# Kernel tuning notes

Measured on AMD Instinct MI355X. Metric: run time of the kernel, lower is better.

The kernel has to match this reference:

```python
import jax, jax.numpy as jnp
import numpy as np

TEMPERATURE = 0.3


def setup_inputs() -> dict:
    key = jax.random.key(0)
    k1, k2, k3 = jax.random.split(key, 3)
    B, C = 65536, 1000
    logits = jax.random.normal(k1, (B, C), dtype=jnp.float32)
    targets = jax.random.randint(k2, (B,), 0, C, dtype=jnp.int64)
    similarity_matrix = jax.random.uniform(k3, (C, C), dtype=jnp.float32)
    return {"logits": logits, "targets": targets, "similarity_matrix": similarity_matrix}


def reference(logits, targets, similarity_matrix):
    # Gather per-sample similarity rows: [B, C]
    sim_rows = similarity_matrix[targets]
    # soft_targets = normalized exp(-sim/T) == softmax(-sim/T) along classes
    soft_targets = jax.nn.softmax(-sim_rows / TEMPERATURE, axis=1)
    log_probs = jax.nn.log_softmax(logits, axis=1)
    loss = -(soft_targets * log_probs).sum(axis=1).mean()
    return loss
```

## Files before the change

kernel.cpp:

```cpp
#include <hip/hip_runtime.h>
#include <math.h>


#define TEMPERATURE 0.3f
#define C_DIM 1000
#define LOSS_BLOCKS 2048

__device__ __forceinline__ float waveAllSum(float v) {
    #pragma unroll
    for (int m = 1; m < 64; m <<= 1) v += __shfl_xor(v, m, 64);
    return v;
}

__global__ void soft_targets_kernel(const float* __restrict__ sim,
                                    float* __restrict__ P) {
    const int wid  = threadIdx.x >> 6;
    const int lane = threadIdx.x & 63;
    const int c = blockIdx.x * 4 + wid;

    const float4* row  = (const float4*)(sim + (size_t)c * C_DIM);
    float4*       prow = (float4*)(P + (size_t)c * C_DIM);

    const bool tail = lane < 58;
    const int  i3   = tail ? lane + 192 : lane;

    float4 v0 = row[lane];
    float4 v1 = row[lane + 64];
    float4 v2 = row[lane + 128];
    float4 v3 = row[i3];

    const float s = -1.0f / TEMPERATURE;
    float4 e0, e1, e2, e3;
    e0.x = __expf(v0.x * s); e0.y = __expf(v0.y * s); e0.z = __expf(v0.z * s); e0.w = __expf(v0.w * s);
    e1.x = __expf(v1.x * s); e1.y = __expf(v1.y * s); e1.z = __expf(v1.z * s); e1.w = __expf(v1.w * s);
    e2.x = __expf(v2.x * s); e2.y = __expf(v2.y * s); e2.z = __expf(v2.z * s); e2.w = __expf(v2.w * s);
    e3.x = __expf(v3.x * s); e3.y = __expf(v3.y * s); e3.z = __expf(v3.z * s); e3.w = __expf(v3.w * s);

    float sum = (e0.x + e0.y + e0.z + e0.w)
              + (e1.x + e1.y + e1.z + e1.w)
              + (e2.x + e2.y + e2.z + e2.w)
              + (tail ? (e3.x + e3.y + e3.z + e3.w) : 0.0f);
    sum = waveAllSum(sum);
    const float inv = 1.0f / sum;

    prow[lane]       = make_float4(e0.x * inv, e0.y * inv, e0.z * inv, e0.w * inv);
    prow[lane + 64]  = make_float4(e1.x * inv, e1.y * inv, e1.z * inv, e1.w * inv);
    prow[lane + 128] = make_float4(e2.x * inv, e2.y * inv, e2.z * inv, e2.w * inv);
    if (tail)
        prow[lane + 192] = make_float4(e3.x * inv, e3.y * inv, e3.z * inv, e3.w * inv);
}

__global__ void loss_kernel(const float* __restrict__ logits,
                            const int* __restrict__ targets,
                            const float* __restrict__ P,
                            float* __restrict__ partials,
                            int B) {
    const int wid  = threadIdx.x >> 6;
    const int lane = threadIdx.x & 63;
    const int wave   = blockIdx.x * 4 + wid;
    const int nwaves = gridDim.x * 4;

    const bool tail = lane < 58;
    const int  i3   = tail ? lane + 192 : lane;

    float local = 0.0f;

    for (int i = wave; i < B; i += nwaves) {
        const int t = targets[i];
        const float4* lrow = (const float4*)(logits + (size_t)i * C_DIM);
        const float4* prow = (const float4*)(P + (size_t)t * C_DIM);

        float4 a0 = lrow[lane];
        float4 a1 = lrow[lane + 64];
        float4 a2 = lrow[lane + 128];
        float4 a3 = lrow[i3];
        float4 p0 = prow[lane];
        float4 p1 = prow[lane + 64];
        float4 p2 = prow[lane + 128];
        float4 p3 = prow[i3];

        float es = (__expf(a0.x) + __expf(a0.y) + __expf(a0.z) + __expf(a0.w))
                 + (__expf(a1.x) + __expf(a1.y) + __expf(a1.z) + __expf(a1.w))
                 + (__expf(a2.x) + __expf(a2.y) + __expf(a2.z) + __expf(a2.w));
        float es3 = __expf(a3.x) + __expf(a3.y) + __expf(a3.z) + __expf(a3.w);

        float dt = a0.x * p0.x + a0.y * p0.y + a0.z * p0.z + a0.w * p0.w
                 + a1.x * p1.x + a1.y * p1.y + a1.z * p1.z + a1.w * p1.w
                 + a2.x * p2.x + a2.y * p2.y + a2.z * p2.z + a2.w * p2.w;
        float dt3 = a3.x * p3.x + a3.y * p3.y + a3.z * p3.z + a3.w * p3.w;

        if (tail) { es += es3; dt += dt3; }

        es = waveAllSum(es);
        dt = waveAllSum(dt);

        local += __logf(es) - dt;
    }

    __shared__ float sloc[4];
    if (lane == 0) sloc[wid] = local;
    __syncthreads();
    if (threadIdx.x == 0)
        partials[blockIdx.x] = sloc[0] + sloc[1] + sloc[2] + sloc[3];
}

__global__ void finalize_kernel(const float* __restrict__ partials,
                                float* __restrict__ out, float invB) {
    const int wid  = threadIdx.x >> 6;
    const int lane = threadIdx.x & 63;
    float v = 0.0f;
    for (int i = threadIdx.x; i < LOSS_BLOCKS; i += 256) v += partials[i];
    v = waveAllSum(v);
    __shared__ float s[4];
    if (lane == 0) s[wid] = v;
    __syncthreads();
    if (threadIdx.x == 0) out[0] = (s[0] + s[1] + s[2] + s[3]) * invB;
}

extern "C" void kernel_launch(void* const* d_in, const int* in_sizes, int n_in,
                              void* d_out, int out_size, void* d_ws, size_t ws_size,
                              hipStream_t stream) {
    const float* logits  = (const float*)d_in[0];
    const int*   targets = (const int*)d_in[1];
    const float* sim     = (const float*)d_in[2];
    float* out = (float*)d_out;

    float* P        = (float*)d_ws;
    float* partials = (float*)d_ws + C_DIM * C_DIM;

    const int B = in_sizes[1];

    soft_targets_kernel<<<250, 256, 0, stream>>>(sim, P);
    loss_kernel<<<LOSS_BLOCKS, 256, 0, stream>>>(logits, targets, P, partials, B);
    finalize_kernel<<<1, 256, 0, stream>>>(partials, out, 1.0f / (float)B);
}
```

Before: 366.1 us.

## Unroll loss loop by two, defer dot reduction, nontemporal logits, atomic finalize

The loss loop now handles two samples per iteration so more loads are in flight. The per-sample dot-product reduction is replaced by one reduction at the end of each wave. Logits are read with nontemporal loads so the similarity-probability table stays cached. The finalize kernel is dropped in favour of an atomicAdd into a memset output, which removes a launch but makes the float summation order nondeterministic.

```diff
diff --git a/kernel.cpp b/kernel.cpp
--- a/kernel.cpp
+++ b/kernel.cpp
@@ -5,6 +5,8 @@
 #define TEMPERATURE 0.3f
 #define C_DIM 1000
 #define LOSS_BLOCKS 2048
+
+typedef float f4 __attribute__((ext_vector_type(4)));
 
 __device__ __forceinline__ float waveAllSum(float v) {
     #pragma unroll
@@ -18,19 +20,19 @@
     const int lane = threadIdx.x & 63;
     const int c = blockIdx.x * 4 + wid;
 
-    const float4* row  = (const float4*)(sim + (size_t)c * C_DIM);
-    float4*       prow = (float4*)(P + (size_t)c * C_DIM);
+    const f4* row  = (const f4*)(sim + (size_t)c * C_DIM);
+    f4*       prow = (f4*)(P + (size_t)c * C_DIM);
 
     const bool tail = lane < 58;
     const int  i3   = tail ? lane + 192 : lane;
 
-    float4 v0 = row[lane];
-    float4 v1 = row[lane + 64];
-    float4 v2 = row[lane + 128];
-    float4 v3 = row[i3];
+    f4 v0 = row[lane];
+    f4 v1 = row[lane + 64];
+    f4 v2 = row[lane + 128];
+    f4 v3 = row[i3];
 
     const float s = -1.0f / TEMPERATURE;
-    float4 e0, e1, e2, e3;
+    f4 e0, e1, e2, e3;
     e0.x = __expf(v0.x * s); e0.y = __expf(v0.y * s); e0.z = __expf(v0.z * s); e0.w = __expf(v0.w * s);
     e1.x = __expf(v1.x * s); e1.y = __expf(v1.y * s); e1.z = __expf(v1.z * s); e1.w = __expf(v1.w * s);
     e2.x = __expf(v2.x * s); e2.y = __expf(v2.y * s); e2.z = __expf(v2.z * s); e2.w = __expf(v2.w * s);
@@ -43,18 +45,48 @@
     sum = waveAllSum(sum);
     const float inv = 1.0f / sum;
 
-    prow[lane]       = make_float4(e0.x * inv, e0.y * inv, e0.z * inv, e0.w * inv);
-    prow[lane + 64]  = make_float4(e1.x * inv, e1.y * inv, e1.z * inv, e1.w * inv);
-    prow[lane + 128] = make_float4(e2.x * inv, e2.y * inv, e2.z * inv, e2.w * inv);
-    if (tail)
-        prow[lane + 192] = make_float4(e3.x * inv, e3.y * inv, e3.z * inv, e3.w * inv);
+    prow[lane]       = e0 * inv;
+    prow[lane + 64]  = e1 * inv;
+    prow[lane + 128] = e2 * inv;
+    if (tail) prow[lane + 192] = e3 * inv;
+}
+
+__device__ __forceinline__ void sample_body(const float* __restrict__ logits,
+                                            const float* __restrict__ P,
+                                            int i, int t, int lane, int i3, bool tail,
+                                            float& es_out, float& acc_dt) {
+    const f4* lrow = (const f4*)(logits + (size_t)i * C_DIM);
+    const f4* prow = (const f4*)(P + (size_t)t * C_DIM);
+
+    f4 a0 = __builtin_nontemporal_load(lrow + lane);
+    f4 a1 = __builtin_nontemporal_load(lrow + lane + 64);
+    f4 a2 = __builtin_nontemporal_load(lrow + lane + 128);
+    f4 a3 = __builtin_nontemporal_load(lrow + i3);
+    f4 p0 = prow[lane];
+    f4 p1 = prow[lane + 64];
+    f4 p2 = prow[lane + 128];
+    f4 p3 = prow[i3];
+
+    float es = (__expf(a0.x) + __expf(a0.y) + __expf(a0.z) + __expf(a0.w))
+             + (__expf(a1.x) + __expf(a1.y) + __expf(a1.z) + __expf(a1.w))
+             + (__expf(a2.x) + __expf(a2.y) + __expf(a2.z) + __expf(a2.w));
+    float es3 = __expf(a3.x) + __expf(a3.y) + __expf(a3.z) + __expf(a3.w);
+
+    float dt = a0.x * p0.x + a0.y * p0.y + a0.z * p0.z + a0.w * p0.w
+             + a1.x * p1.x + a1.y * p1.y + a1.z * p1.z + a1.w * p1.w
+             + a2.x * p2.x + a2.y * p2.y + a2.z * p2.z + a2.w * p2.w;
+    float dt3 = a3.x * p3.x + a3.y * p3.y + a3.z * p3.z + a3.w * p3.w;
+
+    if (tail) { es += es3; dt += dt3; }
+    es_out = es;
+    acc_dt += dt;
 }
 
 __global__ void loss_kernel(const float* __restrict__ logits,
                             const int* __restrict__ targets,
                             const float* __restrict__ P,
-                            float* __restrict__ partials,
-                            int B) {
+                            float* __restrict__ out,
+                            float invB, int B) {
     const int wid  = threadIdx.x >> 6;
     const int lane = threadIdx.x & 63;
     const int wave   = blockIdx.x * 4 + wid;
@@ -63,58 +95,36 @@
     const bool tail = lane < 58;
     const int  i3   = tail ? lane + 192 : lane;
 
-    float local = 0.0f;
+    float acc_log = 0.0f;
+    float acc_dt  = 0.0f;
 
-    for (int i = wave; i < B; i += nwaves) {
+    int i = wave;
+    for (; i + nwaves < B; i += 2 * nwaves) {
+        const int ta = targets[i];
+        const int tb = targets[i + nwaves];
+        float esA, esB;
+        sample_body(logits, P, i,          ta, lane, i3, tail, esA, acc_dt);
+        sample_body(logits, P, i + nwaves, tb, lane, i3, tail, esB, acc_dt);
+        esA = waveAllSum(esA);
+        esB = waveAllSum(esB);
+        acc_log += __logf(esA) + __logf(esB);
+    }
+    for (; i < B; i += nwaves) {
         const int t = targets[i];
-        const float4* lrow = (const float4*)(logits + (size_t)i * C_DIM);
-        const float4* prow = (const float4*)(P + (size_t)t * C_DIM);
-
-        float4 a0 = lrow[lane];
-        float4 a1 = lrow[lane + 64];
-        float4 a2 = lrow[lane + 128];
-        float4 a3 = lrow[i3];
-        float4 p0 = prow[lane];
-        float4 p1 = prow[lane + 64];
-        float4 p2 = prow[lane + 128];
-        float4 p3 = prow[i3];
-
-        float es = (__expf(a0.x) + __expf(a0.y) + __expf(a0.z) + __expf(a0.w))
-                 + (__expf(a1.x) + __expf(a1.y) + __expf(a1.z) + __expf(a1.w))
-                 + (__expf(a2.x) + __expf(a2.y) + __expf(a2.z) + __expf(a2.w));
-        float es3 = __expf(a3.x) + __expf(a3.y) + __expf(a3.z) + __expf(a3.w);
-
-        float dt = a0.x * p0.x + a0.y * p0.y + a0.z * p0.z + a0.w * p0.w
-                 + a1.x * p1.x + a1.y * p1.y + a1.z * p1.z + a1.w * p1.w
-                 + a2.x * p2.x + a2.y * p2.y + a2.z * p2.z + a2.w * p2.w;
-        float dt3 = a3.x * p3.x + a3.y * p3.y + a3.z * p3.z + a3.w * p3.w;
-
-        if (tail) { es += es3; dt += dt3; }
-
+        float es;
+        sample_body(logits, P, i, t, lane, i3, tail, es, acc_dt);
         es = waveAllSum(es);
-        dt = waveAllSum(dt);
-
-        local += __logf(es) - dt;
+        acc_log += __logf(es);
     }
 
+    const float dt_total = waveAllSum(acc_dt);
     __shared__ float sloc[4];
-    if (lane == 0) sloc[wid] = local;
+    if (lane == 0) sloc[wid] = acc_log - dt_total;
     __syncthreads();
-    if (threadIdx.x == 0)
-        partials[blockIdx.x] = sloc[0] + sloc[1] + sloc[2] + sloc[3];
-}
-
-__global__ void finalize_kernel(const float* __restrict__ partials,
-                                float* __restrict__ out, float invB) {
-    const int wid  = threadIdx.x >> 6;
-    const int lane = threadIdx.x & 63;
-    float v = 0.0f;
-    for (int i = threadIdx.x; i < LOSS_BLOCKS; i += 256) v += partials[i];
-    v = waveAllSum(v);
-    __shared__ float s[4];
-    if (lane == 0) s[wid] = v;
-    __syncthreads();
-    if (threadIdx.x == 0) out[0] = (s[0] + s[1] + s[2] + s[3]) * invB;
+    if (threadIdx.x == 0) {
+        const float blk = sloc[0] + sloc[1] + sloc[2] + sloc[3];
+        atomicAdd(out, blk * invB);
+    }
 }
 
 extern "C" void kernel_launch(void* const* d_in, const int* in_sizes, int n_in,
@@ -124,13 +134,12 @@
     const int*   targets = (const int*)d_in[1];
     const float* sim     = (const float*)d_in[2];
     float* out = (float*)d_out;
-
-    float* P        = (float*)d_ws;
-    float* partials = (float*)d_ws + C_DIM * C_DIM;
+    float* P   = (float*)d_ws;
 
     const int B = in_sizes[1];
 
+    hipMemsetAsync(out, 0, sizeof(float), stream);
     soft_targets_kernel<<<250, 256, 0, stream>>>(sim, P);
-    loss_kernel<<<LOSS_BLOCKS, 256, 0, stream>>>(logits, targets, P, partials, B);
-    finalize_kernel<<<1, 256, 0, stream>>>(partials, out, 1.0f / (float)B);
+    loss_kernel<<<LOSS_BLOCKS, 256, 0, stream>>>(logits, targets, P, out,
+                                                 1.0f / (float)B, B);
 }
```

Result: faster. 350.6 us (-4.2%).
